# Kernel tuning notes

Measured on AMD Instinct MI355X. Metric: run time of the kernel, lower is better.

Reference implementation:

```python
import jax, jax.numpy as jnp
import numpy as np

N = 16384      # nodes
E = 131072     # edges
D = 768        # in_size = hid_size = out_size (LayerNorm(768) hardcoded)
NT = 4         # num edge types (TypedLinear num_types)
NB = 3         # num bases (basis regularizer)
LN_EPS = 1e-5


def _layernorm(x, gamma, beta):
    mu = jnp.mean(x, axis=-1, keepdims=True)
    var = jnp.mean(jnp.square(x - mu), axis=-1, keepdims=True)
    return (x - mu) * jax.lax.rsqrt(var + LN_EPS) * gamma + beta


def setup_inputs() -> dict:
    key = jax.random.key(0)
    ks = jax.random.split(key, 16)
    s = 0.02  # weight init scale
    return {
        "h": jax.random.normal(ks[0], (N, D), jnp.float32),
        # TypedLinear basis params: W = sum_b coeff[t,b] * basis[b]
        "W_text": jax.random.normal(ks[1], (NB, D, D), jnp.float32) * s,
        "coeff_text": jax.random.normal(ks[2], (NT, NB), jnp.float32),
        "W_user": jax.random.normal(ks[3], (NB, D, D), jnp.float32) * s,
        "coeff_user": jax.random.normal(ks[4], (NT, NB), jnp.float32),
        "W_dst": jax.random.normal(ks[5], (NB, D, D), jnp.float32) * s,
        "coeff_dst": jax.random.normal(ks[6], (NT, NB), jnp.float32),
        "ln_gamma": jnp.ones((D,), jnp.float32),
        "ln_beta": jnp.zeros((D,), jnp.float32),
        "W_lin": jax.random.normal(ks[7], (2 * D, D), jnp.float32) * s,
        "b_lin": jnp.zeros((D,), jnp.float32),
        "src": jax.random.randint(ks[8], (E,), 0, N, dtype=jnp.int32),
        "dst": jax.random.randint(ks[9], (E,), 0, N, dtype=jnp.int32),
        "etype": jax.random.randint(ks[10], (E,), 0, NT, dtype=jnp.int32),
        "hete": jax.random.randint(ks[11], (E,), 0, 2, dtype=jnp.int32),
    }


def reference(h, W_text, coeff_text, W_user, coeff_user, W_dst, coeff_dst,
              ln_gamma, ln_beta, W_lin, b_lin, src, dst, etype, hete):
    # eval mode: dropout = identity
    x = _layernorm(h, ln_gamma, ln_beta)                       # [N, D]
    # Typed-linear via basis decomposition, folded per (type, node): [NT, N, D]
    Ht = jnp.einsum('nd,bdh,tb->tnh', x, W_text, coeff_text)
    Hu = jnp.einsum('nd,bdh,tb->tnh', x, W_user, coeff_user)
    Hd = jnp.einsum('nd,bdh,tb->tnh', x, W_dst, coeff_dst)

    mask = hete > 0                                            # hete vs homo edges
    # per-edge routed source message: [E, D]
    ef = jnp.where(mask[:, None],
                   jax.nn.relu(Ht[etype, src]),
                   jax.nn.relu(Hu[etype, src]))
    # Original concatenates [hete_feat, homo_feat] along edge dim, i.e. a stable
    # permutation putting hete edges first; dst features stay in original order.
    perm = jnp.argsort((~mask).astype(jnp.int32), stable=True)
    feat_perm = ef[perm]                                       # [E, D]
    dfeat = jax.nn.relu(Hd[etype, dst])                        # [E, D]
    m = jnp.concatenate([feat_perm, dfeat], axis=-1)           # [E, 2D]
    # scatter-sum messages to destination nodes
    n = jax.ops.segment_sum(m, dst, num_segments=N)            # [N, 2D]
    z = jax.nn.relu(n @ W_lin + b_lin)                         # [N, D]
    zn = jnp.linalg.norm(z, ord=2, axis=1, keepdims=True)
    zn = jnp.where(zn == 0, jnp.asarray(1.0, z.dtype), zn)
    return z / zn
```

## Files before the change

kernel.cpp:

```cpp
#include <hip/hip_runtime.h>
#include <hip/hip_bf16.h>
#include <cstdint>

static constexpr int N_  = 16384;
static constexpr int E_  = 131072;
static constexpr int D_  = 768;
static constexpr int D2_ = 1536;
static constexpr int DSQ_ = D_ * D_;

static constexpr size_t OFF_XB   = 0;
static constexpr size_t OFF_WBT  = 25165824;
static constexpr size_t OFF_WLT  = 39321600;
static constexpr size_t OFF_NB16 = 41680896;
static constexpr size_t OFF_Y3   = 92012544;
static constexpr size_t OFF_ZB   = 92012544;
static constexpr size_t OFF_N1C  = 192675840;
static constexpr size_t OFF_TG   = 217841664;
static constexpr size_t OFF_PAY  = 218365952;
static constexpr size_t OFF_CNT  = 218890240;
static constexpr size_t OFF_BASE = 219152384;
static constexpr size_t OFF_CUR  = 219217936;
static constexpr size_t OFF_BC   = 219283472;
static constexpr size_t OFF_SCAN = 219285520;

typedef __attribute__((ext_vector_type(8))) short short8v;
typedef __attribute__((ext_vector_type(4))) float floatx4;

__device__ __forceinline__ void gld16(const void* g, void* l) {
  __builtin_amdgcn_global_load_lds(
      (const __attribute__((address_space(1))) unsigned int*)g,
      (__attribute__((address_space(3))) unsigned int*)l, 16, 0, 0);
}

__device__ __forceinline__ float b2f(short u) {
  union { unsigned int i; float f; } x;
  x.i = ((unsigned int)(unsigned short)u) << 16;
  return x.f;
}

__device__ __forceinline__ float wave_sum(float v) {
#pragma unroll
  for (int o = 32; o; o >>= 1) v += __shfl_down(v, o, 64);
  return v;
}

__global__ __launch_bounds__(256) void wbasis_t_kernel(
    const float* __restrict__ Wt, const float* __restrict__ Wu,
    const float* __restrict__ Wd, __hip_bfloat16* __restrict__ WbT) {
  __shared__ float tile[64][65];
  int fb = blockIdx.y;
  int f = fb / 3, b = fb % 3;
  const float* W = ((f == 0) ? Wt : ((f == 1) ? Wu : Wd)) + (size_t)b * DSQ_;
  int dt = (blockIdx.x / 12) * 64;
  int ht = (blockIdx.x % 12) * 64;
  int tid = threadIdx.x;
#pragma unroll
  for (int jj = 0; jj < 16; jj++) {
    int idx = jj * 256 + tid;
    int rr = idx >> 6, cc = idx & 63;
    tile[rr][cc] = W[(size_t)(dt + rr) * D_ + ht + cc];
  }
  __syncthreads();
#pragma unroll
  for (int jj = 0; jj < 16; jj++) {
    int idx = jj * 256 + tid;
    int hh = idx >> 6, dd = idx & 63;
    WbT[(size_t)fb * DSQ_ + (size_t)(ht + hh) * D_ + dt + dd] =
        __float2bfloat16(tile[dd][hh]);
  }
}

__global__ __launch_bounds__(256) void wlint_kernel(
    const float* __restrict__ W, __hip_bfloat16* __restrict__ WT) {
  int i = blockIdx.x * 256 + threadIdx.x;
  int k = i / D_, h = i % D_;
  WT[(size_t)h * D2_ + k] = __float2bfloat16(W[i]);
}

__global__ __launch_bounds__(256) void ln_kernel(
    const float* __restrict__ h, const float* __restrict__ gamma,
    const float* __restrict__ beta, __hip_bfloat16* __restrict__ x) {
  int v = blockIdx.x, tid = threadIdx.x;
  const float* hr = h + (size_t)v * D_;
  float e0 = hr[tid], e1 = hr[tid + 256], e2 = hr[tid + 512];
  float s = e0 + e1 + e2;
  float q = e0 * e0 + e1 * e1 + e2 * e2;
  __shared__ float red[8];
  __shared__ float mv[2];
  float ws_ = wave_sum(s), wq = wave_sum(q);
  int lane = tid & 63, w = tid >> 6;
  if (lane == 0) { red[w] = ws_; red[4 + w] = wq; }
  __syncthreads();
  if (tid == 0) {
    float S = red[0] + red[1] + red[2] + red[3];
    float Q = red[4] + red[5] + red[6] + red[7];
    float mu = S * (1.0f / D_);
    float var = Q * (1.0f / D_) - mu * mu;
    mv[0] = mu;
    mv[1] = rsqrtf(var + 1e-5f);
  }
  __syncthreads();
  float mu = mv[0], rstd = mv[1];
  __hip_bfloat16* xr = x + (size_t)v * D_;
  xr[tid]       = __float2bfloat16((e0 - mu) * rstd * gamma[tid]       + beta[tid]);
  xr[tid + 256] = __float2bfloat16((e1 - mu) * rstd * gamma[tid + 256] + beta[tid + 256]);
  xr[tid + 512] = __float2bfloat16((e2 - mu) * rstd * gamma[tid + 512] + beta[tid + 512]);
}

__global__ __launch_bounds__(256) void edge_a_kernel(
    const int* __restrict__ hete, const int* __restrict__ dst,
    const int* __restrict__ etype, int* __restrict__ blockcnt,
    int* __restrict__ cnt4) {
  int j = blockIdx.x * 256 + threadIdx.x;
  int flag = hete[j] > 0;
  unsigned long long m = __ballot(flag);
  __shared__ int wsum[4];
  int lane = threadIdx.x & 63, w = threadIdx.x >> 6;
  if (lane == 0) wsum[w] = __popcll(m);
  __syncthreads();
  if (threadIdx.x == 0)
    blockcnt[blockIdx.x] = wsum[0] + wsum[1] + wsum[2] + wsum[3];
  atomicAdd(&cnt4[dst[j] * 4 + etype[j]], 1);
}

__global__ __launch_bounds__(512) void scan_kernel(
    const int* __restrict__ blockcnt, int* __restrict__ scanout) {
  __shared__ int s[512];
  int t = threadIdx.x;
  int v = blockcnt[t];
  s[t] = v;
  __syncthreads();
  for (int o = 1; o < 512; o <<= 1) {
    int add = (t >= o) ? s[t - o] : 0;
    __syncthreads();
    s[t] += add;
    __syncthreads();
  }
  scanout[t] = s[t] - v;
  if (t == 511) scanout[512] = s[511];
}

__global__ __launch_bounds__(256) void edge_b_kernel(
    const int* __restrict__ hete, const int* __restrict__ dst,
    const int* __restrict__ scanout, int* __restrict__ target) {
  int j = blockIdx.x * 256 + threadIdx.x;
  int flag = hete[j] > 0;
  unsigned long long m = __ballot(flag);
  __shared__ int wsum[4];
  int lane = threadIdx.x & 63, w = threadIdx.x >> 6;
  if (lane == 0) wsum[w] = __popcll(m);
  __syncthreads();
  int wpre = 0;
#pragma unroll
  for (int i = 0; i < 4; i++) wpre += (i < w) ? wsum[i] : 0;
  int lpre = __popcll(m & ((1ull << lane) - 1ull));
  int hcum = scanout[blockIdx.x] + wpre + lpre;
  int K = scanout[512];
  int e = flag ? hcum : (K + j - hcum);
  target[j] = dst[e];
}

__global__ __launch_bounds__(1024) void base_scan_kernel(
    const int* __restrict__ cnt4, int* __restrict__ base) {
  __shared__ int s[1024];
  int t = threadIdx.x;
  int loc[16];
  int sum = 0;
#pragma unroll
  for (int i = 0; i < 16; i++) {
    int v = t * 16 + i;
    int d = cnt4[v * 4] + cnt4[v * 4 + 1] + cnt4[v * 4 + 2] + cnt4[v * 4 + 3];
    loc[i] = sum;
    sum += d;
  }
  s[t] = sum;
  __syncthreads();
  for (int o = 1; o < 1024; o <<= 1) {
    int add = (t >= o) ? s[t - o] : 0;
    __syncthreads();
    s[t] += add;
    __syncthreads();
  }
  int pre = t ? s[t - 1] : 0;
#pragma unroll
  for (int i = 0; i < 16; i++) base[t * 16 + i] = pre + loc[i];
  if (t == 1023) base[N_] = s[1023];
}

__global__ __launch_bounds__(256) void edge_sort_kernel(
    const int* __restrict__ target, const int* __restrict__ src,
    const int* __restrict__ etype, const int* __restrict__ hete,
    const int* __restrict__ base, int* __restrict__ cursor,
    int* __restrict__ payload) {
  int j = blockIdx.x * 256 + threadIdx.x;
  int v = target[j];
  int p = base[v] + atomicAdd(&cursor[v], 1);
  int g = ((hete[j] > 0) ? 0 : 4) + etype[j];
  payload[p] = (g << 14) | src[j];
}

template <bool FIRST>
__global__ __launch_bounds__(256) void gather_n1_kernel(
    const __hip_bfloat16* __restrict__ Y, const float* __restrict__ coeff,
    const int* __restrict__ base, const int* __restrict__ payload,
    __hip_bfloat16* __restrict__ n1c, __hip_bfloat16* __restrict__ nb16,
    int g0) {
  int wv = threadIdx.x >> 6, lane = threadIdx.x & 63;
  int v = blockIdx.x * 4 + wv;
  int b0 = base[v], b1 = base[v + 1];
  float cf[12];
#pragma unroll
  for (int i = 0; i < 12; i++) cf[i] = coeff[i];
  float acc[12];
  if (FIRST) {
#pragma unroll
    for (int i = 0; i < 12; i++) acc[i] = 0.f;
  } else {
    short8v a8 = *(const short8v*)(n1c + (size_t)v * D_ + lane * 8);
    short4  b4 = *(const short4*)(n1c + (size_t)v * D_ + 512 + lane * 4);
#pragma unroll
    for (int i = 0; i < 8; i++) acc[i] = b2f(a8[i]);
    acc[8] = b2f(b4.x); acc[9] = b2f(b4.y);
    acc[10] = b2f(b4.z); acc[11] = b2f(b4.w);
  }
  const size_t YS = (size_t)N_ * D_;
  for (int idx = b0; idx < b1; ++idx) {
    int pl = payload[idx];
    int t = (pl >> 14) - g0;
    if ((unsigned)t > 3u) continue;
    float c0 = cf[t * 3], c1 = cf[t * 3 + 1], c2 = cf[t * 3 + 2];
    const __hip_bfloat16* r0 = Y + (size_t)(pl & 16383) * D_;
    short8v a0 = *(const short8v*)(r0 + lane * 8);
    short8v a1 = *(const short8v*)(r0 + YS + lane * 8);
    short8v a2 = *(const short8v*)(r0 + 2 * YS + lane * 8);
    short4  b0v = *(const short4*)(r0 + 512 + lane * 4);
    short4  b1v = *(const short4*)(r0 + YS + 512 + lane * 4);
    short4  b2v = *(const short4*)(r0 + 2 * YS + 512 + lane * 4);
#pragma unroll
    for (int i = 0; i < 8; i++)
      acc[i] += fmaxf(c0 * b2f(a0[i]) + c1 * b2f(a1[i]) + c2 * b2f(a2[i]), 0.f);
    acc[8]  += fmaxf(c0 * b2f(b0v.x) + c1 * b2f(b1v.x) + c2 * b2f(b2v.x), 0.f);
    acc[9]  += fmaxf(c0 * b2f(b0v.y) + c1 * b2f(b1v.y) + c2 * b2f(b2v.y), 0.f);
    acc[10] += fmaxf(c0 * b2f(b0v.z) + c1 * b2f(b1v.z) + c2 * b2f(b2v.z), 0.f);
    acc[11] += fmaxf(c0 * b2f(b0v.w) + c1 * b2f(b1v.w) + c2 * b2f(b2v.w), 0.f);
  }
  __hip_bfloat16 o[12];
#pragma unroll
  for (int i = 0; i < 12; i++) o[i] = __float2bfloat16(acc[i]);
  if (FIRST) {
    *(short8v*)(n1c + (size_t)v * D_ + lane * 8) = *(const short8v*)o;
    *(short4*)(n1c + (size_t)v * D_ + 512 + lane * 4) = *(const short4*)(o + 8);
  } else {
    *(short8v*)(nb16 + (size_t)v * D2_ + lane * 8) = *(const short8v*)o;
    *(short4*)(nb16 + (size_t)v * D2_ + 512 + lane * 4) = *(const short4*)(o + 8);
  }
}

__global__ __launch_bounds__(256) void combine_n2_kernel(
    const __hip_bfloat16* __restrict__ Y, const float* __restrict__ cd,
    const int* __restrict__ cnt4, __hip_bfloat16* __restrict__ nb16) {
  size_t i = ((size_t)blockIdx.x * 256 + threadIdx.x) * 8;
  int v = (int)(i / D_);
  int k = (int)(i % D_);
  const size_t YS = (size_t)N_ * D_;
  short8v y0 = *(const short8v*)(Y + i);
  short8v y1 = *(const short8v*)(Y + YS + i);
  short8v y2 = *(const short8v*)(Y + 2 * YS + i);
  float f0[8], f1[8], f2[8];
#pragma unroll
  for (int j = 0; j < 8; j++) {
    f0[j] = b2f(y0[j]); f1[j] = b2f(y1[j]); f2[j] = b2f(y2[j]);
  }
  float acc[8] = {0.f, 0.f, 0.f, 0.f, 0.f, 0.f, 0.f, 0.f};
#pragma unroll
  for (int t = 0; t < 4; t++) {
    float c = (float)cnt4[v * 4 + t];
    if (c != 0.f) {
      float d0 = cd[t * 3], d1 = cd[t * 3 + 1], d2 = cd[t * 3 + 2];
#pragma unroll
      for (int j = 0; j < 8; j++)
        acc[j] += c * fmaxf(d0 * f0[j] + d1 * f1[j] + d2 * f2[j], 0.f);
    }
  }
  __hip_bfloat16 o[8];
#pragma unroll
  for (int j = 0; j < 8; j++) o[j] = __float2bfloat16(acc[j]);
  *(short8v*)(nb16 + (size_t)v * D2_ + D_ + k) = *(const short8v*)o;
}

template <bool BIAS, bool RELU>
__global__ __launch_bounds__(256) void gemm_mfma_kernel(
    const __hip_bfloat16* __restrict__ A, const __hip_bfloat16* __restrict__ BT0,
    const float* __restrict__ bias, __hip_bfloat16* __restrict__ C0,
    int M, int N, int K, size_t strideB, size_t strideC) {
  __shared__ char lds[32768];
  char* As = lds;
  char* Bs = lds + 16384;
  int tid = threadIdx.x;
  int lane = tid & 63;
  int wv = tid >> 6;
  int wr = wv >> 1, wc = wv & 1;
  int gx = gridDim.x, gz = gridDim.z;
  int nwg = gx * gridDim.y * gz;
  int id = (blockIdx.z * gridDim.y + blockIdx.y) * gx + blockIdx.x;
  int s = (id & 7) * (nwg >> 3) + (id >> 3);
  int bx = s % gx;
  int rem = s / gx;
  int z = rem % gz;
  int by = rem / gz;
  const __hip_bfloat16* BT = BT0 + (size_t)z * strideB;
  int row0 = by * 128, col0 = bx * 128;
  int r_ = tid >> 3;
  int s_ = tid & 7;

  floatx4 acc[4][4];
#pragma unroll
  for (int i = 0; i < 4; i++)
#pragma unroll
    for (int j = 0; j < 4; j++) acc[i][j] = floatx4{0.f, 0.f, 0.f, 0.f};

  for (int k0 = 0; k0 < K; k0 += 64) {
    __syncthreads();
#pragma unroll
    for (int is = 0; is < 4; is++) {
      int r = is * 32 + r_;
      int sp = s_ ^ (r & 7);
      gld16(A  + (size_t)(row0 + r) * K + k0 + sp * 8, As + is * 4096 + tid * 16);
      gld16(BT + (size_t)(col0 + r) * K + k0 + sp * 8, Bs + is * 4096 + tid * 16);
    }
    __syncthreads();
#pragma unroll
    for (int kk = 0; kk < 64; kk += 32) {
      int p = (kk >> 3) + (lane >> 4);
      short8v af[4], bf[4];
#pragma unroll
      for (int m = 0; m < 4; m++) {
        int ra = wr * 64 + m * 16 + (lane & 15);
        af[m] = *(const short8v*)(As + ra * 128 + ((p ^ (ra & 7)) << 4));
        int rb = wc * 64 + m * 16 + (lane & 15);
        bf[m] = *(const short8v*)(Bs + rb * 128 + ((p ^ (rb & 7)) << 4));
      }
#pragma unroll
      for (int m = 0; m < 4; m++)
#pragma unroll
        for (int n = 0; n < 4; n++)
          acc[m][n] = __builtin_amdgcn_mfma_f32_16x16x32_bf16(
              af[m], bf[n], acc[m][n], 0, 0, 0);
    }
  }
  __syncthreads();
  char* cs = lds + wv * 8192;
#pragma unroll
  for (int m = 0; m < 4; m++) {
#pragma unroll
    for (int n = 0; n < 4; n++) {
      int c = n * 16 + (lane & 15);
      float bv = BIAS ? bias[col0 + wc * 64 + c] : 0.f;
#pragma unroll
      for (int q = 0; q < 4; q++) {
        int r = m * 16 + (lane >> 4) * 4 + q;
        float v = acc[m][n][q] + bv;
        if (RELU) v = fmaxf(v, 0.f);
        int byte = r * 128 + ((((c >> 3) + r) & 7) << 4) + ((c & 7) << 1);
        *(__hip_bfloat16*)(cs + byte) = __float2bfloat16(v);
      }
    }
  }
  __hip_bfloat16* C = C0 + (size_t)z * strideC;
#pragma unroll
  for (int i = 0; i < 8; i++) {
    int r = i * 8 + (lane >> 3);
    int s8 = lane & 7;
    int p = (s8 + r) & 7;
    short8v v = *(const short8v*)(cs + r * 128 + (p << 4));
    int grow = row0 + wr * 64 + r;
    int gcol = col0 + wc * 64 + s8 * 8;
    *(short8v*)(C + (size_t)grow * N + gcol) = v;
  }
}

__global__ __launch_bounds__(256) void norm_kernel(
    const __hip_bfloat16* __restrict__ z, float* __restrict__ out) {
  int v = blockIdx.x, tid = threadIdx.x;
  float e[4] = {0.f, 0.f, 0.f, 0.f};
  if (tid < 192) {
    short4 a = *(const short4*)(z + (size_t)v * D_ + tid * 4);
    e[0] = b2f(a.x); e[1] = b2f(a.y); e[2] = b2f(a.z); e[3] = b2f(a.w);
  }
  float q = e[0] * e[0] + e[1] * e[1] + e[2] * e[2] + e[3] * e[3];
  __shared__ float red[4];
  __shared__ float sc;
  float wq = wave_sum(q);
  int lane = tid & 63, w = tid >> 6;
  if (lane == 0) red[w] = wq;
  __syncthreads();
  if (tid == 0) {
    float S = red[0] + red[1] + red[2] + red[3];
    float norm = sqrtf(S);
    sc = (norm == 0.f) ? 1.f : (1.f / norm);
  }
  __syncthreads();
  if (tid < 192) {
    float s = sc;
    float4 o = {e[0] * s, e[1] * s, e[2] * s, e[3] * s};
    *(float4*)(out + (size_t)v * D_ + tid * 4) = o;
  }
}

extern "C" void kernel_launch(void* const* d_in, const int* in_sizes, int n_in,
                              void* d_out, int out_size, void* d_ws,
                              size_t ws_size, hipStream_t stream) {
  (void)in_sizes; (void)n_in; (void)out_size; (void)ws_size;
  const float* h      = (const float*)d_in[0];
  const float* W_text = (const float*)d_in[1];
  const float* c_text = (const float*)d_in[2];
  const float* W_user = (const float*)d_in[3];
  const float* c_user = (const float*)d_in[4];
  const float* W_dst  = (const float*)d_in[5];
  const float* c_dst  = (const float*)d_in[6];
  const float* gamma  = (const float*)d_in[7];
  const float* beta   = (const float*)d_in[8];
  const float* W_lin  = (const float*)d_in[9];
  const float* b_lin  = (const float*)d_in[10];
  const int* src      = (const int*)d_in[11];
  const int* dst      = (const int*)d_in[12];
  const int* etype    = (const int*)d_in[13];
  const int* hete     = (const int*)d_in[14];
  float* out          = (float*)d_out;

  char* ws = (char*)d_ws;
  __hip_bfloat16* xb   = (__hip_bfloat16*)(ws + OFF_XB);
  __hip_bfloat16* WbT  = (__hip_bfloat16*)(ws + OFF_WBT);
  __hip_bfloat16* WlT  = (__hip_bfloat16*)(ws + OFF_WLT);
  __hip_bfloat16* nb16 = (__hip_bfloat16*)(ws + OFF_NB16);
  __hip_bfloat16* Y3   = (__hip_bfloat16*)(ws + OFF_Y3);
  __hip_bfloat16* zbuf = (__hip_bfloat16*)(ws + OFF_ZB);
  __hip_bfloat16* n1c  = (__hip_bfloat16*)(ws + OFF_N1C);
  int* target   = (int*)(ws + OFF_TG);
  int* payload  = (int*)(ws + OFF_PAY);
  int* cnt4     = (int*)(ws + OFF_CNT);
  int* base     = (int*)(ws + OFF_BASE);
  int* cursor   = (int*)(ws + OFF_CUR);
  int* blockcnt = (int*)(ws + OFF_BC);
  int* scanout  = (int*)(ws + OFF_SCAN);

  hipMemsetAsync(cnt4, 0, (size_t)N_ * 4 * 4, stream);
  hipMemsetAsync(cursor, 0, (size_t)N_ * 4, stream);

  wbasis_t_kernel<<<dim3(144, 9), 256, 0, stream>>>(W_text, W_user, W_dst, WbT);
  wlint_kernel<<<(D2_ * D_) / 256, 256, 0, stream>>>(W_lin, WlT);
  ln_kernel<<<N_, 256, 0, stream>>>(h, gamma, beta, xb);
  edge_a_kernel<<<E_ / 256, 256, 0, stream>>>(hete, dst, etype, blockcnt, cnt4);
  scan_kernel<<<1, 512, 0, stream>>>(blockcnt, scanout);
  edge_b_kernel<<<E_ / 256, 256, 0, stream>>>(hete, dst, scanout, target);
  base_scan_kernel<<<1, 1024, 0, stream>>>(cnt4, base);
  edge_sort_kernel<<<E_ / 256, 256, 0, stream>>>(target, src, etype, hete,
                                                 base, cursor, payload);

  const size_t HSTRIDE = (size_t)N_ * D_;
  const dim3 ggrid(D_ / 128, N_ / 128, 3);

  gemm_mfma_kernel<false, false><<<ggrid, 256, 0, stream>>>(
      xb, WbT + (size_t)6 * DSQ_, nullptr, Y3, N_, D_, D_, DSQ_, HSTRIDE);
  combine_n2_kernel<<<(N_ * D_) / (256 * 8), 256, 0, stream>>>(Y3, c_dst,
                                                               cnt4, nb16);
  gemm_mfma_kernel<false, false><<<ggrid, 256, 0, stream>>>(
      xb, WbT, nullptr, Y3, N_, D_, D_, DSQ_, HSTRIDE);
  gather_n1_kernel<true><<<N_ / 4, 256, 0, stream>>>(Y3, c_text, base, payload,
                                                     n1c, nb16, 0);
  gemm_mfma_kernel<false, false><<<ggrid, 256, 0, stream>>>(
      xb, WbT + (size_t)3 * DSQ_, nullptr, Y3, N_, D_, D_, DSQ_, HSTRIDE);
  gather_n1_kernel<false><<<N_ / 4, 256, 0, stream>>>(Y3, c_user, base,
                                                      payload, n1c, nb16, 4);

  gemm_mfma_kernel<true, true><<<dim3(D_ / 128, N_ / 128, 1), 256, 0, stream>>>(
      nb16, WlT, b_lin, zbuf, N_, D_, D2_, 0, 0);
  norm_kernel<<<N_, 256, 0, stream>>>(zbuf, out);
}
```

Before: 478.4 us.

## Fuse edge preprocessing kernels and split CSR segments by hete flag

Merges the two scans into one two-block kernel and fuses the target computation with the edge bucket sort, dropping the intermediate target array and two launches. Each destination's CSR segment is filled from both ends, hete edges from the front and homo edges from the back, so each gather pass walks only its own edges instead of scanning all of them and skipping by type. The memsets are merged into one contiguous clear. The cost is an extra cursor array, and the payload order within a segment changes, which can alter bf16 accumulation order.

```diff
diff --git a/kernel.cpp b/kernel.cpp
--- a/kernel.cpp
+++ b/kernel.cpp
@@ -15,13 +15,13 @@
 static constexpr size_t OFF_Y3   = 92012544;
 static constexpr size_t OFF_ZB   = 92012544;
 static constexpr size_t OFF_N1C  = 192675840;
-static constexpr size_t OFF_TG   = 217841664;
-static constexpr size_t OFF_PAY  = 218365952;
-static constexpr size_t OFF_CNT  = 218890240;
-static constexpr size_t OFF_BASE = 219152384;
-static constexpr size_t OFF_CUR  = 219217936;
-static constexpr size_t OFF_BC   = 219283472;
-static constexpr size_t OFF_SCAN = 219285520;
+static constexpr size_t OFF_PAY  = 217841664;
+static constexpr size_t OFF_CNT  = 218365952;
+static constexpr size_t OFF_CURH = 218628096;
+static constexpr size_t OFF_CURU = 218693632;
+static constexpr size_t OFF_BASE = 218759168;
+static constexpr size_t OFF_BC   = 218824736;
+static constexpr size_t OFF_SCAN = 218826784;
 
 typedef __attribute__((ext_vector_type(8))) short short8v;
 typedef __attribute__((ext_vector_type(4))) float floatx4;
@@ -123,26 +123,55 @@
   atomicAdd(&cnt4[dst[j] * 4 + etype[j]], 1);
 }
 
-__global__ __launch_bounds__(512) void scan_kernel(
-    const int* __restrict__ blockcnt, int* __restrict__ scanout) {
-  __shared__ int s[512];
+__global__ __launch_bounds__(1024) void fused_scan_kernel(
+    const int* __restrict__ blockcnt, int* __restrict__ scanout,
+    const int* __restrict__ cnt4, int* __restrict__ base) {
   int t = threadIdx.x;
-  int v = blockcnt[t];
-  s[t] = v;
-  __syncthreads();
-  for (int o = 1; o < 512; o <<= 1) {
-    int add = (t >= o) ? s[t - o] : 0;
+  if (blockIdx.x == 0) {
+    __shared__ int s[1024];
+    int v = (t < 512) ? blockcnt[t] : 0;
+    s[t] = v;
     __syncthreads();
-    s[t] += add;
+    for (int o = 1; o < 512; o <<= 1) {
+      int add = (t >= o) ? s[t - o] : 0;
+      __syncthreads();
+      s[t] += add;
+      __syncthreads();
+    }
+    if (t < 512) scanout[t] = s[t] - v;
+    if (t == 511) scanout[512] = s[511];
+  } else {
+    __shared__ int s[1024];
+    int loc[16];
+    int sum = 0;
+#pragma unroll
+    for (int i = 0; i < 16; i++) {
+      int v = t * 16 + i;
+      int d = cnt4[v * 4] + cnt4[v * 4 + 1] + cnt4[v * 4 + 2] + cnt4[v * 4 + 3];
+      loc[i] = sum;
+      sum += d;
+    }
+    s[t] = sum;
     __syncthreads();
-  }
-  scanout[t] = s[t] - v;
-  if (t == 511) scanout[512] = s[511];
-}
-
-__global__ __launch_bounds__(256) void edge_b_kernel(
+    for (int o = 1; o < 1024; o <<= 1) {
+      int add = (t >= o) ? s[t - o] : 0;
+      __syncthreads();
+      s[t] += add;
+      __syncthreads();
+    }
+    int pre = t ? s[t - 1] : 0;
+#pragma unroll
+    for (int i = 0; i < 16; i++) base[t * 16 + i] = pre + loc[i];
+    if (t == 1023) base[N_] = s[1023];
+  }
+}
+
+__global__ __launch_bounds__(256) void edge_bsort_kernel(
     const int* __restrict__ hete, const int* __restrict__ dst,
-    const int* __restrict__ scanout, int* __restrict__ target) {
+    const int* __restrict__ src, const int* __restrict__ etype,
+    const int* __restrict__ scanout, const int* __restrict__ base,
+    int* __restrict__ curH, int* __restrict__ curU,
+    int* __restrict__ payload) {
   int j = blockIdx.x * 256 + threadIdx.x;
   int flag = hete[j] > 0;
   unsigned long long m = __ballot(flag);
@@ -157,57 +186,24 @@
   int hcum = scanout[blockIdx.x] + wpre + lpre;
   int K = scanout[512];
   int e = flag ? hcum : (K + j - hcum);
-  target[j] = dst[e];
-}
-
-__global__ __launch_bounds__(1024) void base_scan_kernel(
-    const int* __restrict__ cnt4, int* __restrict__ base) {
-  __shared__ int s[1024];
-  int t = threadIdx.x;
-  int loc[16];
-  int sum = 0;
-#pragma unroll
-  for (int i = 0; i < 16; i++) {
-    int v = t * 16 + i;
-    int d = cnt4[v * 4] + cnt4[v * 4 + 1] + cnt4[v * 4 + 2] + cnt4[v * 4 + 3];
-    loc[i] = sum;
-    sum += d;
-  }
-  s[t] = sum;
-  __syncthreads();
-  for (int o = 1; o < 1024; o <<= 1) {
-    int add = (t >= o) ? s[t - o] : 0;
-    __syncthreads();
-    s[t] += add;
-    __syncthreads();
-  }
-  int pre = t ? s[t - 1] : 0;
-#pragma unroll
-  for (int i = 0; i < 16; i++) base[t * 16 + i] = pre + loc[i];
-  if (t == 1023) base[N_] = s[1023];
-}
-
-__global__ __launch_bounds__(256) void edge_sort_kernel(
-    const int* __restrict__ target, const int* __restrict__ src,
-    const int* __restrict__ etype, const int* __restrict__ hete,
-    const int* __restrict__ base, int* __restrict__ cursor,
-    int* __restrict__ payload) {
-  int j = blockIdx.x * 256 + threadIdx.x;
-  int v = target[j];
-  int p = base[v] + atomicAdd(&cursor[v], 1);
-  int g = ((hete[j] > 0) ? 0 : 4) + etype[j];
-  payload[p] = (g << 14) | src[j];
-}
-
-template <bool FIRST>
+  int v = dst[e];
+  int p;
+  if (flag) p = base[v] + atomicAdd(&curH[v], 1);
+  else      p = base[v + 1] - 1 - atomicAdd(&curU[v], 1);
+  payload[p] = (etype[j] << 14) | src[j];
+}
+
+template <bool FIRST, int SEG>
 __global__ __launch_bounds__(256) void gather_n1_kernel(
     const __hip_bfloat16* __restrict__ Y, const float* __restrict__ coeff,
-    const int* __restrict__ base, const int* __restrict__ payload,
-    __hip_bfloat16* __restrict__ n1c, __hip_bfloat16* __restrict__ nb16,
-    int g0) {
+    const int* __restrict__ base, const int* __restrict__ hcnt,
+    const int* __restrict__ payload, __hip_bfloat16* __restrict__ n1c,
+    __hip_bfloat16* __restrict__ nb16) {
   int wv = threadIdx.x >> 6, lane = threadIdx.x & 63;
   int v = blockIdx.x * 4 + wv;
-  int b0 = base[v], b1 = base[v + 1];
+  int bh = base[v] + hcnt[v];
+  int lo = (SEG == 0) ? base[v] : bh;
+  int hi = (SEG == 0) ? bh : base[v + 1];
   float cf[12];
 #pragma unroll
   for (int i = 0; i < 12; i++) cf[i] = coeff[i];
@@ -224,10 +220,9 @@
     acc[10] = b2f(b4.z); acc[11] = b2f(b4.w);
   }
   const size_t YS = (size_t)N_ * D_;
-  for (int idx = b0; idx < b1; ++idx) {
+  for (int idx = lo; idx < hi; ++idx) {
     int pl = payload[idx];
-    int t = (pl >> 14) - g0;
-    if ((unsigned)t > 3u) continue;
+    int t = pl >> 14;
     float c0 = cf[t * 3], c1 = cf[t * 3 + 1], c2 = cf[t * 3 + 2];
     const __hip_bfloat16* r0 = Y + (size_t)(pl & 16383) * D_;
     short8v a0 = *(const short8v*)(r0 + lane * 8);
@@ -436,26 +431,24 @@
   __hip_bfloat16* Y3   = (__hip_bfloat16*)(ws + OFF_Y3);
   __hip_bfloat16* zbuf = (__hip_bfloat16*)(ws + OFF_ZB);
   __hip_bfloat16* n1c  = (__hip_bfloat16*)(ws + OFF_N1C);
-  int* target   = (int*)(ws + OFF_TG);
   int* payload  = (int*)(ws + OFF_PAY);
   int* cnt4     = (int*)(ws + OFF_CNT);
+  int* curH     = (int*)(ws + OFF_CURH);
+  int* curU     = (int*)(ws + OFF_CURU);
   int* base     = (int*)(ws + OFF_BASE);
-  int* cursor   = (int*)(ws + OFF_CUR);
   int* blockcnt = (int*)(ws + OFF_BC);
   int* scanout  = (int*)(ws + OFF_SCAN);
 
-  hipMemsetAsync(cnt4, 0, (size_t)N_ * 4 * 4, stream);
-  hipMemsetAsync(cursor, 0, (size_t)N_ * 4, stream);
+  hipMemsetAsync(cnt4, 0, 262144 + 65536 + 65536, stream);
 
   wbasis_t_kernel<<<dim3(144, 9), 256, 0, stream>>>(W_text, W_user, W_dst, WbT);
   wlint_kernel<<<(D2_ * D_) / 256, 256, 0, stream>>>(W_lin, WlT);
   ln_kernel<<<N_, 256, 0, stream>>>(h, gamma, beta, xb);
   edge_a_kernel<<<E_ / 256, 256, 0, stream>>>(hete, dst, etype, blockcnt, cnt4);
-  scan_kernel<<<1, 512, 0, stream>>>(blockcnt, scanout);
-  edge_b_kernel<<<E_ / 256, 256, 0, stream>>>(hete, dst, scanout, target);
-  base_scan_kernel<<<1, 1024, 0, stream>>>(cnt4, base);
-  edge_sort_kernel<<<E_ / 256, 256, 0, stream>>>(target, src, etype, hete,
-                                                 base, cursor, payload);
+  fused_scan_kernel<<<2, 1024, 0, stream>>>(blockcnt, scanout, cnt4, base);
+  edge_bsort_kernel<<<E_ / 256, 256, 0, stream>>>(hete, dst, src, etype,
+                                                  scanout, base, curH, curU,
+                                                  payload);
 
   const size_t HSTRIDE = (size_t)N_ * D_;
   const dim3 ggrid(D_ / 128, N_ / 128, 3);
@@ -466,12 +459,12 @@
                                                                cnt4, nb16);
   gemm_mfma_kernel<false, false><<<ggrid, 256, 0, stream>>>(
       xb, WbT, nullptr, Y3, N_, D_, D_, DSQ_, HSTRIDE);
-  gather_n1_kernel<true><<<N_ / 4, 256, 0, stream>>>(Y3, c_text, base, payload,
-                                                     n1c, nb16, 0);
+  gather_n1_kernel<true, 0><<<N_ / 4, 256, 0, stream>>>(
+      Y3, c_text, base, curH, payload, n1c, nb16);
   gemm_mfma_kernel<false, false><<<ggrid, 256, 0, stream>>>(
       xb, WbT + (size_t)3 * DSQ_, nullptr, Y3, N_, D_, D_, DSQ_, HSTRIDE);
-  gather_n1_kernel<false><<<N_ / 4, 256, 0, stream>>>(Y3, c_user, base,
-                                                      payload, n1c, nb16, 4);
+  gather_n1_kernel<false, 1><<<N_ / 4, 256, 0, stream>>>(
+      Y3, c_user, base, curH, payload, n1c, nb16);
 
   gemm_mfma_kernel<true, true><<<dim3(D_ / 128, N_ / 128, 1), 256, 0, stream>>>(
       nb16, WlT, b_lin, zbuf, N_, D_, D2_, 0, 0);
```

After: 470.3 us. About the same (-1.7%).
